# Optimization experiments

Hardware: AMD Instinct MI355X
Metric: run time of the kernel (lower is better)

## Reference

```python
import jax, jax.numpy as jnp
import numpy as np

T, N, NH, H, R, E = 6, 50000, 128, 4, 2, 800000
D = NH // H


def _pos_enc(d, t):
    # matches HTHGNLayer TempAttention.generate_positional_encoding
    k = np.arange(0, d, 2)
    div = np.exp(k * -np.log(100000.0) / d)
    pos = np.arange(1, t + 1)[:, None].astype(np.float64)
    pe = np.zeros((t, d), dtype=np.float32)
    pe[:, 0::2] = np.sin(pos * div)
    pe[:, 1::2] = np.cos(pos * div)
    return jnp.asarray(pe)


def setup_inputs() -> dict:
    key = jax.random.key(0)
    ks = jax.random.split(key, 16)
    s = 1.0 / np.sqrt(NH)  # keep activations / attention logits well-scaled
    inp = {
        "x": jax.random.normal(ks[0], (T, N, NH), jnp.float32),
        "src": jax.random.randint(ks[1], (R, E), 0, N, jnp.int32),
        "dst": jax.random.randint(ks[2], (R, E), 0, N, jnp.int32),
        "gat_wsrc": jax.random.normal(ks[3], (R, NH, NH), jnp.float32) * s,
        "gat_wdst": jax.random.normal(ks[4], (R, NH, NH), jnp.float32) * s,
        "gat_attn": jax.random.normal(ks[5], (R, H, D), jnp.float32) * s,
        "gat_bias": jnp.zeros((R, NH), jnp.float32),
        "h_bias": jnp.zeros((NH,), jnp.float32),
        "sem_w1": jax.random.normal(ks[6], (NH, NH), jnp.float32) * s,
        "sem_b1": jnp.zeros((NH,), jnp.float32),
        "sem_w2": jax.random.normal(ks[7], (NH,), jnp.float32) * s,
        "proj_w": jax.random.normal(ks[8], (NH, NH), jnp.float32) * s,
        "proj_b": jnp.zeros((NH,), jnp.float32),
        "qw": jax.random.normal(ks[9], (NH, NH), jnp.float32) * s,
        "kw": jax.random.normal(ks[10], (NH, NH), jnp.float32) * s,
        "vw": jax.random.normal(ks[11], (NH, NH), jnp.float32) * s,
        "fc_w": jax.random.normal(ks[12], (NH, NH), jnp.float32) * s,
        "fc_b": jnp.zeros((NH,), jnp.float32),
        "res_w": jax.random.normal(ks[13], (NH, NH), jnp.float32) * s,
        "res_b": jnp.zeros((NH,), jnp.float32),
        "res_alpha": jax.random.normal(ks[14], (1,), jnp.float32),
        "ln_gamma": jnp.ones((NH,), jnp.float32),
        "ln_beta": jnp.zeros((NH,), jnp.float32),
    }
    return inp


def _gatv2_rel(xt, s_, d_, wsrc, wdst, attn, bias):
    # one relation, one timestep: DGL GATv2Conv (share_weights=False, slope 0.2)
    fs = (xt @ wsrc).reshape(N, H, D)  # fc_src
    fd = (xt @ wdst).reshape(N, H, D)  # fc_dst
    e = jax.nn.leaky_relu(fs[s_] + fd[d_], 0.2)           # [E,H,D]
    sc = jnp.einsum('ehd,hd->eh', e, attn)                # [E,H]
    m = jax.ops.segment_max(sc, d_, num_segments=N)       # edge softmax per dst
    ex = jnp.exp(sc - m[d_])
    den = jax.ops.segment_sum(ex, d_, num_segments=N)
    alpha = ex / den[d_]
    out = jax.ops.segment_sum(alpha[:, :, None] * fs[s_], d_, num_segments=N)
    return out + bias.reshape(1, H, D)                    # [N,H,D]


def reference(x, src, dst, gat_wsrc, gat_wdst, gat_attn, gat_bias, h_bias,
              sem_w1, sem_b1, sem_w2, proj_w, proj_b, qw, kw, vw, fc_w, fc_b,
              res_w, res_b, res_alpha, ln_gamma, ln_beta):
    gat_all = jax.vmap(_gatv2_rel, in_axes=(None, 0, 0, 0, 0, 0, 0))
    inter = []
    for t in range(T):  # fixed small time window
        hr = gat_all(x[t], src, dst, gat_wsrc, gat_wdst, gat_attn, gat_bias)  # [R,N,H,D]
        h = jnp.transpose(hr, (1, 0, 2, 3)).reshape(N, R, NH)  # stack + flatten heads
        # semantic attention over relations (_rel_agg)
        w = jnp.tanh(h @ sem_w1 + sem_b1) @ sem_w2             # [N,R]
        beta = jax.nn.softmax(w.mean(0), axis=0)               # [R]
        hsem = jax.nn.relu(jnp.einsum('r,nrd->nd', beta, h))
        inter.append(jax.nn.relu(hsem + h_bias))               # _apply: bias + relu
    inter = jnp.stack(inter, 0)                                # [T,N,NH]
    # temporal self-attention (TempAttention, no 1/sqrt(d) scaling -- faithful)
    pe = _pos_enc(NH, T)
    xt = jnp.transpose(inter, (1, 0, 2))                       # [N,T,NH]
    hh = xt @ proj_w + proj_b + pe
    q, k, v = hh @ qw, hh @ kw, hh @ vw
    sc = jax.nn.softmax(jnp.einsum('ntd,nsd->nts', q, k), axis=-1)
    ho = jax.nn.relu(jnp.einsum('nts,nsd->ntd', sc, v) @ fc_w + fc_b)
    ho = jnp.transpose(ho, (1, 0, 2))                          # [T,N,NH]
    # gated residual + LayerNorm
    a = jax.nn.sigmoid(res_alpha)[0]
    out = ho * a + (x @ res_w + res_b) * (1.0 - a)
    mu = out.mean(-1, keepdims=True)
    var = out.var(-1, keepdims=True)
    return (out - mu) / jnp.sqrt(var + 1e-5) * ln_gamma + ln_beta
```

## Files before the change

kernel.cpp:

```cpp
#include <hip/hip_runtime.h>
#include <math.h>

#define T_  6
#define N_  50000
#define NH_ 128
#define R_  2
#define E_  800000
#define SEMW_BLOCKS ((2*N_ + 127)/128)

typedef __attribute__((ext_vector_type(8))) short bf16x8;
typedef __attribute__((ext_vector_type(4))) float f32x4;

__device__ inline unsigned short f2b(float f) {
    union { float f; unsigned int u; } v; v.f = f;
    unsigned int u = v.u;
    unsigned int r = (u + 0x7FFFu + ((u >> 16) & 1u)) >> 16;
    return (unsigned short)r;
}
__device__ inline float b2f(unsigned short h) {
    union { unsigned int u; float f; } v; v.u = ((unsigned int)h) << 16;
    return v.f;
}

__global__ void hist_kernel(const int* __restrict__ dst, int* __restrict__ counts) {
    int j = blockIdx.x * blockDim.x + threadIdx.x;
    if (j < R_ * E_) atomicAdd(&counts[(j / E_) * N_ + dst[j]], 1);
}

__global__ __launch_bounds__(1024) void scan_kernel(const int* __restrict__ counts,
                                                    int* __restrict__ offsets,
                                                    int* __restrict__ cursor) {
    int r = blockIdx.x;
    __shared__ int sm[1024];
    __shared__ int carry;
    if (threadIdx.x == 0) carry = 0;
    __syncthreads();
    for (int base = 0; base < N_; base += 1024) {
        int i = base + threadIdx.x;
        int v = (i < N_) ? counts[r * N_ + i] : 0;
        sm[threadIdx.x] = v;
        __syncthreads();
        for (int off = 1; off < 1024; off <<= 1) {
            int t = 0;
            if (threadIdx.x >= off) t = sm[threadIdx.x - off];
            __syncthreads();
            sm[threadIdx.x] += t;
            __syncthreads();
        }
        int incl = sm[threadIdx.x];
        int run = carry;
        int excl = run + incl - v;
        if (i < N_) { offsets[r * (N_ + 1) + i] = excl; cursor[r * N_ + i] = excl; }
        __syncthreads();
        if (threadIdx.x == 1023) carry = run + incl;
        __syncthreads();
    }
    if (threadIdx.x == 0) offsets[r * (N_ + 1) + N_] = carry;
}

__global__ void scatter_kernel(const int* __restrict__ src, const int* __restrict__ dst,
                               int* __restrict__ cursor, int* __restrict__ srcs_sorted) {
    int j = blockIdx.x * blockDim.x + threadIdx.x;
    if (j < R_ * E_) {
        int r = j / E_;
        int pos = atomicAdd(&cursor[r * N_ + dst[j]], 1);
        srcs_sorted[(size_t)r * E_ + pos] = src[j];
    }
}

__global__ void pe_kernel(float* __restrict__ pe) {
    int c = threadIdx.x;
    int k = c & ~1;
    double div = exp((double)k * (-log(100000.0) / 128.0));
    for (int t = 0; t < T_; t++) {
        double pos = (double)(t + 1);
        double v = (c & 1) ? cos(pos * div) : sin(pos * div);
        pe[t * NH_ + c] = (float)v;
    }
}

__global__ void cvt_x_kernel(const float* __restrict__ in, unsigned short* __restrict__ out, long n) {
    long i = ((long)blockIdx.x * blockDim.x + threadIdx.x) * 8;
    if (i >= n) return;
    float4 a = *(const float4*)(in + i);
    float4 b = *(const float4*)(in + i + 4);
    union { unsigned short s[8]; uint4 u; } o;
    o.s[0] = f2b(a.x); o.s[1] = f2b(a.y); o.s[2] = f2b(a.z); o.s[3] = f2b(a.w);
    o.s[4] = f2b(b.x); o.s[5] = f2b(b.y); o.s[6] = f2b(b.z); o.s[7] = f2b(b.w);
    *(uint4*)(out + i) = o.u;
}

struct CvtArgs {
    const float* s[6];
    unsigned short* d[6];
};
__global__ void cvt_wt_kernel(CvtArgs a) {
    int y = blockIdx.y, n = blockIdx.x, k = threadIdx.x;
    a.d[y][n * 128 + k] = f2b(a.s[y][k * 128 + n]);
}

__global__ void build_m_kernel(const float* __restrict__ qw, const float* __restrict__ kw,
                               const float* __restrict__ vw, const float* __restrict__ fcw,
                               float* __restrict__ Mu, float* __restrict__ Mwv) {
    int y = blockIdx.y, c = blockIdx.x, f = threadIdx.x;
    float s = 0.f;
    if (y == 0) {
        for (int d = 0; d < 128; d++) s += kw[f * 128 + d] * qw[c * 128 + d];
        Mu[c * 128 + f] = s;
    } else {
        for (int d = 0; d < 128; d++) s += vw[f * 128 + d] * fcw[d * 128 + c];
        Mwv[c * 128 + f] = s;
    }
}

__global__ void fold_w_kernel(const float* __restrict__ proj, const float* __restrict__ Mu,
                              const float* __restrict__ Mwv, unsigned short* __restrict__ wt_hh,
                              unsigned short* __restrict__ wt_pu, unsigned short* __restrict__ wt_pwv) {
    int y = blockIdx.y, c = blockIdx.x, k = threadIdx.x;
    if (y == 0) { wt_hh[c * 128 + k] = f2b(proj[k * 128 + c]); return; }
    const float* M = (y == 1) ? Mu : Mwv;
    float s = 0.f;
    for (int f = 0; f < 128; f++) s += proj[k * 128 + f] * M[c * 128 + f];
    ((y == 1) ? wt_pu : wt_pwv)[c * 128 + k] = f2b(s);
}

__global__ void fold_c_kernel(const float* __restrict__ proj_b, const float* __restrict__ pe,
                              const float* __restrict__ Mu, const float* __restrict__ Mwv,
                              const float* __restrict__ res_b, float* __restrict__ cbuf) {
    int t = blockIdx.x, c = threadIdx.x;
    cbuf[0 * 768 + t * 128 + c] = proj_b[c] + pe[t * 128 + c];
    float s1 = 0.f, s2 = 0.f;
    for (int f = 0; f < 128; f++) {
        float b = proj_b[f] + pe[t * 128 + f];
        s1 += b * Mu[c * 128 + f];
        s2 += b * Mwv[c * 128 + f];
    }
    cbuf[1 * 768 + t * 128 + c] = s1;
    cbuf[2 * 768 + t * 128 + c] = s2;
    cbuf[3 * 768 + t * 128 + c] = res_b[c];
}

struct MArgs {
    const unsigned short* A;
    const unsigned short* Axb;
    const unsigned short* W0; const unsigned short* W1;
    const unsigned short* W2; const unsigned short* W3;
    unsigned short* C0; unsigned short* C1; unsigned short* C2; unsigned short* C3;
    const float* cb;
    long row0;
    int  M;
};

template <int EPI>
__global__ __launch_bounds__(256) void mgemm_kernel(MArgs g) {
    __shared__ __align__(16) char As[128 * 256];
    __shared__ __align__(16) char Bs[128 * 256];
    int tid = threadIdx.x;
    int brow0 = blockIdx.x * 128;
    const unsigned short* Ws[4] = {g.W0, g.W1, g.W2, g.W3};
    unsigned short* Cs[4] = {g.C0, g.C1, g.C2, g.C3};

    auto stageA = [&](const unsigned short* Abase, bool m1) {
#pragma unroll
        for (int i = 0; i < 8; i++) {
            int c = tid + i * 256;
            int row = c >> 4;
            int cb = (c & 15) << 4;
            int scb = cb ^ ((row & 7) << 4);
            int grow = brow0 + row;
            float4 av = make_float4(0.f, 0.f, 0.f, 0.f);
            if (grow < g.M) {
                long ar;
                if (!m1) ar = grow;
                else { long gg = g.row0 + grow; long n = gg / 6, t = gg - n * 6; ar = t * (long)N_ + n; }
                av = *(const float4*)((const char*)Abase + ar * 256 + cb);
            }
            *(float4*)(As + row * 256 + scb) = av;
        }
    };
    auto stageB = [&](const unsigned short* W) {
#pragma unroll
        for (int i = 0; i < 8; i++) {
            int c = tid + i * 256;
            int row = c >> 4;
            int cb = (c & 15) << 4;
            int scb = cb ^ ((row & 7) << 4);
            *(float4*)(Bs + row * 256 + scb) = *(const float4*)((const char*)W + (size_t)row * 256 + cb);
        }
    };

    int w = tid >> 6, l = tid & 63;
    int l15 = l & 15, lg = l >> 4;

    stageA(g.A, false);
    for (int y = 0; y < 4; y++) {
        if (y > 0) __syncthreads();
        if (EPI == 3 && y == 3) stageA(g.Axb, true);
        stageB(Ws[y]);
        __syncthreads();

        f32x4 acc[2][8];
#pragma unroll
        for (int a = 0; a < 2; a++)
#pragma unroll
            for (int b = 0; b < 8; b++) acc[a][b] = (f32x4)(0.f);
#pragma unroll
        for (int ks = 0; ks < 4; ks++) {
            bf16x8 bf[8];
#pragma unroll
            for (int nt = 0; nt < 8; nt++) {
                int rn = nt * 16 + l15;
                int cbyte = (ks * 64 + lg * 16) ^ ((rn & 7) << 4);
                bf[nt] = *(const bf16x8*)(Bs + rn * 256 + cbyte);
            }
#pragma unroll
            for (int mt = 0; mt < 2; mt++) {
                int rm = w * 32 + mt * 16 + l15;
                int cbyte = (ks * 64 + lg * 16) ^ ((rm & 7) << 4);
                bf16x8 af = *(const bf16x8*)(As + rm * 256 + cbyte);
#pragma unroll
                for (int nt = 0; nt < 8; nt++)
                    acc[mt][nt] = __builtin_amdgcn_mfma_f32_16x16x32_bf16(af, bf[nt], acc[mt][nt], 0, 0, 0);
            }
        }
        unsigned short* C = Cs[y];
#pragma unroll
        for (int mt = 0; mt < 2; mt++) {
#pragma unroll
            for (int r = 0; r < 4; r++) {
                int row = w * 32 + mt * 16 + lg * 4 + r;
                int grow = brow0 + row;
                if (grow >= g.M) continue;
                long t6 = 0;
                if (EPI == 3) t6 = (g.row0 + grow) % 6;
#pragma unroll
                for (int nt = 0; nt < 8; nt++) {
                    int col = nt * 16 + l15;
                    float v = acc[mt][nt][r];
                    if (EPI == 3) v += g.cb[y * 768 + t6 * 128 + col];
                    C[(size_t)grow * 128 + col] = f2b(v);
                }
            }
        }
    }
}

__global__ __launch_bounds__(256) void semw_kernel(const unsigned short* __restrict__ Abase,
                                                   const unsigned short* __restrict__ Wt,
                                                   const float* __restrict__ b1,
                                                   const float* __restrict__ w2,
                                                   float* __restrict__ partials) {
    __shared__ __align__(16) char As[128 * 256];
    __shared__ __align__(16) char Bs[128 * 256];
    __shared__ float bs[2];
    int tid = threadIdx.x;
    if (tid < 2) bs[tid] = 0.f;
    int tl = blockIdx.y;
    const unsigned short* A = Abase + (size_t)tl * N_ * 256;
    const int M = 2 * N_;
    int brow0 = blockIdx.x * 128;
#pragma unroll
    for (int i = 0; i < 8; i++) {
        int c = tid + i * 256;
        int row = c >> 4;
        int cb = (c & 15) << 4;
        int scb = cb ^ ((row & 7) << 4);
        *(float4*)(Bs + row * 256 + scb) = *(const float4*)((const char*)Wt + (size_t)row * 256 + cb);
        int grow = brow0 + row;
        float4 av = make_float4(0.f, 0.f, 0.f, 0.f);
        if (grow < M) av = *(const float4*)((const char*)A + (size_t)grow * 256 + cb);
        *(float4*)(As + row * 256 + scb) = av;
    }
    __syncthreads();
    int w = tid >> 6, l = tid & 63;
    int l15 = l & 15, lg = l >> 4;
    f32x4 acc[2][8];
#pragma unroll
    for (int a = 0; a < 2; a++)
#pragma unroll
        for (int b = 0; b < 8; b++) acc[a][b] = (f32x4)(0.f);
#pragma unroll
    for (int ks = 0; ks < 4; ks++) {
        bf16x8 bf[8];
#pragma unroll
        for (int nt = 0; nt < 8; nt++) {
            int rn = nt * 16 + l15;
            int cbyte = (ks * 64 + lg * 16) ^ ((rn & 7) << 4);
            bf[nt] = *(const bf16x8*)(Bs + rn * 256 + cbyte);
        }
#pragma unroll
        for (int mt = 0; mt < 2; mt++) {
            int rm = w * 32 + mt * 16 + l15;
            int cbyte = (ks * 64 + lg * 16) ^ ((rm & 7) << 4);
            bf16x8 af = *(const bf16x8*)(As + rm * 256 + cbyte);
#pragma unroll
            for (int nt = 0; nt < 8; nt++)
                acc[mt][nt] = __builtin_amdgcn_mfma_f32_16x16x32_bf16(af, bf[nt], acc[mt][nt], 0, 0, 0);
        }
    }
#pragma unroll
    for (int mt = 0; mt < 2; mt++) {
#pragma unroll
        for (int r = 0; r < 4; r++) {
            int row = w * 32 + mt * 16 + lg * 4 + r;
            int grow = brow0 + row;
            float s = 0.f;
#pragma unroll
            for (int nt = 0; nt < 8; nt++) {
                int col = nt * 16 + l15;
                s += tanhf(acc[mt][nt][r] + b1[col]) * w2[col];
            }
#pragma unroll
            for (int mask = 1; mask <= 8; mask <<= 1) s += __shfl_xor(s, mask);
            if (l15 == 0 && grow < M) atomicAdd(&bs[grow & 1], s);
        }
    }
    __syncthreads();
    if (tid < 2) partials[((size_t)tl * SEMW_BLOCKS + blockIdx.x) * 2 + tid] = bs[tid];
}

__global__ __launch_bounds__(512) void beta_kernel(const float* __restrict__ partials,
                                                   float* __restrict__ beta2) {
    int t = blockIdx.x;
    const float* p = partials + (size_t)t * SEMW_BLOCKS * 2;
    float s0 = 0.f, s1 = 0.f;
    for (int i = threadIdx.x; i < SEMW_BLOCKS; i += 512) { s0 += p[i * 2]; s1 += p[i * 2 + 1]; }
#pragma unroll
    for (int mask = 1; mask <= 32; mask <<= 1) { s0 += __shfl_xor(s0, mask); s1 += __shfl_xor(s1, mask); }
    __shared__ float w0[8], w1[8];
    int w = threadIdx.x >> 6;
    if ((threadIdx.x & 63) == 0) { w0[w] = s0; w1[w] = s1; }
    __syncthreads();
    if (threadIdx.x == 0) {
        float t0 = 0.f, t1 = 0.f;
        for (int i = 0; i < 8; i++) { t0 += w0[i]; t1 += w1[i]; }
        float m0 = t0 / (float)N_, m1 = t1 / (float)N_;
        float mx = fmaxf(m0, m1);
        float e0 = __expf(m0 - mx), e1 = __expf(m1 - mx);
        float inv = 1.f / (e0 + e1);
        beta2[t * 2] = e0 * inv; beta2[t * 2 + 1] = e1 * inv;
    }
}

__global__ __launch_bounds__(256) void gat_edge_kernel(const unsigned short* __restrict__ R0,
                                                       const int* __restrict__ offsets,
                                                       const int* __restrict__ srcs_sorted,
                                                       const float* __restrict__ gat_attn,
                                                       const float* __restrict__ gat_bias,
                                                       unsigned short* __restrict__ hbuf, int TB) {
    int y = blockIdx.y;
    int r = y & 1, tl = y >> 1;
    const unsigned short* fs = R0 + ((size_t)(2 * r) * TB + tl) * N_ * 128;
    const unsigned short* fd = R0 + ((size_t)(2 * r + 1) * TB + tl) * N_ * 128;
    unsigned short* hout = hbuf + (size_t)tl * N_ * 256;
    const int* offs = offsets + r * (N_ + 1);
    const int* srcs = srcs_sorted + (size_t)r * E_;
    int lane = threadIdx.x & 63;
    int q = lane >> 4, l16 = lane & 15;
    int c0 = l16 * 8;
    int wid = (blockIdx.x * blockDim.x + threadIdx.x) >> 6;
    int nw = (gridDim.x * blockDim.x) >> 6;
    float4 a0 = *(const float4*)(gat_attn + r * 128 + c0);
    float4 a1 = *(const float4*)(gat_attn + r * 128 + c0 + 4);
    float av[8] = {a0.x, a0.y, a0.z, a0.w, a1.x, a1.y, a1.z, a1.w};
    float4 bb0 = *(const float4*)(gat_bias + r * 128 + c0);
    float4 bb1 = *(const float4*)(gat_bias + r * 128 + c0 + 4);
    float bv[8] = {bb0.x, bb0.y, bb0.z, bb0.w, bb1.x, bb1.y, bb1.z, bb1.w};

    for (int gidx = wid; gidx < N_ / 4; gidx += nw) {
        int n = gidx * 4 + q;
        uint4 fdp = *(const uint4*)(fd + (size_t)n * 128 + c0);
        const unsigned int* fdu = (const unsigned int*)&fdp;
        float fdv[8];
#pragma unroll
        for (int j = 0; j < 8; j++)
            fdv[j] = (j & 1) ? b2f((unsigned short)(fdu[j >> 1] >> 16)) : b2f((unsigned short)fdu[j >> 1]);
        int e0 = offs[n], e1 = offs[n + 1];
        int deg = e1 - e0;
        int m = deg;
        m = max(m, __shfl_xor(m, 16));
        m = max(m, __shfl_xor(m, 32));
        float den = 0.f;
        float acc[8];
#pragma unroll
        for (int j = 0; j < 8; j++) acc[j] = 0.f;

        uint4 fp = make_uint4(0, 0, 0, 0);
        if (deg > 0) fp = *(const uint4*)(fs + (size_t)srcs[e0] * 128 + c0);
        for (int i = 0; i < m; i++) {
            uint4 nxt = make_uint4(0, 0, 0, 0);
            if (i + 1 < deg) nxt = *(const uint4*)(fs + (size_t)srcs[e0 + i + 1] * 128 + c0);
            const unsigned int* fu = (const unsigned int*)&fp;
            float f[8];
            float v = 0.f;
#pragma unroll
            for (int j = 0; j < 8; j++) {
                f[j] = (j & 1) ? b2f((unsigned short)(fu[j >> 1] >> 16)) : b2f((unsigned short)fu[j >> 1]);
                float t = f[j] + fdv[j];
                float lr = fmaf(0.2f, fminf(t, 0.f), fmaxf(t, 0.f));
                v = fmaf(av[j], lr, v);
            }
            v += __int_as_float(__builtin_amdgcn_ds_swizzle(__float_as_int(v), 0x041F));
            v += __int_as_float(__builtin_amdgcn_ds_swizzle(__float_as_int(v), 0x081F));
            float p = (i < deg) ? __expf(v) : 0.f;
            den += p;
#pragma unroll
            for (int j = 0; j < 8; j++) acc[j] = fmaf(p, f[j], acc[j]);
            fp = nxt;
        }
        float inv = (deg > 0) ? 1.f / den : 0.f;
        union { unsigned short s[8]; uint4 u; } o;
#pragma unroll
        for (int j = 0; j < 8; j++) o.s[j] = f2b(fmaf(acc[j], inv, bv[j]));
        *(uint4*)(hout + (size_t)(n * 2 + r) * 128 + c0) = o.u;
    }
}

__global__ void hsem_kernel(const unsigned short* __restrict__ hbuf, const float* __restrict__ beta2,
                            const float* __restrict__ h_bias, unsigned short* __restrict__ inter,
                            int tbase) {
    int idx = blockIdx.x * blockDim.x + threadIdx.x;
    if (idx >= N_ * 16) return;
    int tl = blockIdx.y;
    int t = tbase + tl;
    const unsigned short* h = hbuf + (size_t)tl * N_ * 256;
    int n = idx >> 4, c8 = (idx & 15) * 8;
    float b0 = beta2[tl * 2], b1 = beta2[tl * 2 + 1];
    uint4 x0 = *(const uint4*)(h + (size_t)n * 256 + c8);
    uint4 x1 = *(const uint4*)(h + (size_t)n * 256 + 128 + c8);
    const unsigned int* p0 = (const unsigned int*)&x0;
    const unsigned int* p1 = (const unsigned int*)&x1;
    float4 hb0 = *(const float4*)(h_bias + c8);
    float4 hb1 = *(const float4*)(h_bias + c8 + 4);
    float hbv[8] = {hb0.x, hb0.y, hb0.z, hb0.w, hb1.x, hb1.y, hb1.z, hb1.w};
    union { unsigned short s[8]; uint4 u; } o;
#pragma unroll
    for (int i = 0; i < 8; i++) {
        unsigned short s0 = (i & 1) ? (unsigned short)(p0[i >> 1] >> 16) : (unsigned short)p0[i >> 1];
        unsigned short s1 = (i & 1) ? (unsigned short)(p1[i >> 1] >> 16) : (unsigned short)p1[i >> 1];
        float z = fmaxf(fmaxf(b0 * b2f(s0) + b1 * b2f(s1), 0.f) + hbv[i], 0.f);
        o.s[i] = f2b(z);
    }
    *(uint4*)(inter + ((size_t)n * 6 + t) * 128 + c8) = o.u;
}

__global__ __launch_bounds__(256) void temporal_kernel(const unsigned short* __restrict__ hh,
                                                       const unsigned short* __restrict__ uu,
                                                       const unsigned short* __restrict__ wvv,
                                                       const unsigned short* __restrict__ rv,
                                                       const float* __restrict__ fc_b,
                                                       const float* __restrict__ res_alpha,
                                                       const float* __restrict__ ln_g,
                                                       const float* __restrict__ ln_b,
                                                       float* __restrict__ out, long n0, int nNodes) {
    int lane = threadIdx.x & 63;
    int wid = (blockIdx.x * blockDim.x + threadIdx.x) >> 6;
    if (wid >= nNodes) return;
    long n = n0 + wid;
    size_t base = (size_t)wid * 6 * 128 + 2 * lane;
    float h2[6][2], u2[6][2], wv2[6][2], rv2[6][2];
#pragma unroll
    for (int t = 0; t < 6; t++) {
        unsigned int hp = *(const unsigned int*)(hh + base + t * 128);
        h2[t][0] = b2f((unsigned short)hp); h2[t][1] = b2f((unsigned short)(hp >> 16));
        unsigned int up = *(const unsigned int*)(uu + base + t * 128);
        u2[t][0] = b2f((unsigned short)up); u2[t][1] = b2f((unsigned short)(up >> 16));
        unsigned int wp = *(const unsigned int*)(wvv + base + t * 128);
        wv2[t][0] = b2f((unsigned short)wp); wv2[t][1] = b2f((unsigned short)(wp >> 16));
        unsigned int rp = *(const unsigned int*)(rv + base + t * 128);
        rv2[t][0] = b2f((unsigned short)rp); rv2[t][1] = b2f((unsigned short)(rp >> 16));
    }
    float sc[6][6];
#pragma unroll
    for (int t = 0; t < 6; t++)
#pragma unroll
        for (int s = 0; s < 6; s++)
            sc[t][s] = h2[t][0] * u2[s][0] + h2[t][1] * u2[s][1];
#pragma unroll
    for (int mask = 1; mask <= 32; mask <<= 1)
#pragma unroll
        for (int t = 0; t < 6; t++)
#pragma unroll
            for (int s = 0; s < 6; s++)
                sc[t][s] += __shfl_xor(sc[t][s], mask);

    float a = 1.f / (1.f + __expf(-res_alpha[0]));
    float2 fb = ((const float2*)fc_b)[lane];
    float2 lg = ((const float2*)ln_g)[lane];
    float2 lb = ((const float2*)ln_b)[lane];
#pragma unroll
    for (int t = 0; t < 6; t++) {
        float mx = sc[t][0];
#pragma unroll
        for (int s = 1; s < 6; s++) mx = fmaxf(mx, sc[t][s]);
        float p[6]; float den = 0.f;
#pragma unroll
        for (int s = 0; s < 6; s++) { p[s] = __expf(sc[t][s] - mx); den += p[s]; }
        float inv = 1.f / den;
        float ox = 0.f, oy = 0.f;
#pragma unroll
        for (int s = 0; s < 6; s++) { ox += p[s] * wv2[s][0]; oy += p[s] * wv2[s][1]; }
        ox = fmaxf(ox * inv + fb.x, 0.f);
        oy = fmaxf(oy * inv + fb.y, 0.f);
        ox = ox * a + rv2[t][0] * (1.f - a);
        oy = oy * a + rv2[t][1] * (1.f - a);
        float s1 = ox + oy, s2 = ox * ox + oy * oy;
#pragma unroll
        for (int mask = 1; mask <= 32; mask <<= 1) {
            s1 += __shfl_xor(s1, mask);
            s2 += __shfl_xor(s2, mask);
        }
        float mu = s1 * (1.f / 128.f);
        float var = s2 * (1.f / 128.f) - mu * mu;
        float rs = rsqrtf(var + 1e-5f);
        float2 o;
        o.x = (ox - mu) * rs * lg.x + lb.x;
        o.y = (oy - mu) * rs * lg.y + lb.y;
        ((float2*)(out + ((size_t)t * N_ + n) * 128))[lane] = o;
    }
}

extern "C" void kernel_launch(void* const* d_in, const int* in_sizes, int n_in,
                              void* d_out, int out_size, void* d_ws, size_t ws_size,
                              hipStream_t stream) {
    const float* x        = (const float*)d_in[0];
    const int*   src      = (const int*)d_in[1];
    const int*   dst      = (const int*)d_in[2];
    const float* gat_wsrc = (const float*)d_in[3];
    const float* gat_wdst = (const float*)d_in[4];
    const float* gat_attn = (const float*)d_in[5];
    const float* gat_bias = (const float*)d_in[6];
    const float* h_bias   = (const float*)d_in[7];
    const float* sem_w1   = (const float*)d_in[8];
    const float* sem_b1   = (const float*)d_in[9];
    const float* sem_w2   = (const float*)d_in[10];
    const float* proj_w   = (const float*)d_in[11];
    const float* proj_b   = (const float*)d_in[12];
    const float* qw       = (const float*)d_in[13];
    const float* kw       = (const float*)d_in[14];
    const float* vw       = (const float*)d_in[15];
    const float* fc_w     = (const float*)d_in[16];
    const float* fc_b     = (const float*)d_in[17];
    const float* res_w    = (const float*)d_in[18];
    const float* res_b    = (const float*)d_in[19];
    const float* res_alpha= (const float*)d_in[20];
    const float* ln_g     = (const float*)d_in[21];
    const float* ln_b     = (const float*)d_in[22];
    (void)in_sizes; (void)n_in; (void)out_size;

    int TB = (ws_size >= (size_t)500 * 1024 * 1024) ? 6 : 2;
    int CH = (TB == 6) ? N_ : 12500;

    char* ws = (char*)d_ws;
    size_t off = 0;
    auto alloc = [&](size_t bytes) -> void* {
        void* p = ws + off;
        off += (bytes + 255) & ~(size_t)255;
        return p;
    };
    int*   counts      = (int*)alloc((size_t)R_ * N_ * 4);
    int*   offsets     = (int*)alloc((size_t)R_ * (N_ + 1) * 4);
    int*   cursor      = (int*)alloc((size_t)R_ * N_ * 4);
    int*   srcs_sorted = (int*)alloc((size_t)R_ * E_ * 4);
    float* pe          = (float*)alloc(T_ * NH_ * 4);
    float* partials    = (float*)alloc((size_t)T_ * SEMW_BLOCKS * 2 * 4);
    float* beta2       = (float*)alloc(T_ * 2 * 4);
    float* Mu          = (float*)alloc(16384 * 4);
    float* Mwv         = (float*)alloc(16384 * 4);
    float* cbuf        = (float*)alloc(4 * 768 * 4);
    unsigned short* wt_gs0  = (unsigned short*)alloc(16384 * 2);
    unsigned short* wt_gs1  = (unsigned short*)alloc(16384 * 2);
    unsigned short* wt_gd0  = (unsigned short*)alloc(16384 * 2);
    unsigned short* wt_gd1  = (unsigned short*)alloc(16384 * 2);
    unsigned short* wt_sem  = (unsigned short*)alloc(16384 * 2);
    unsigned short* wt_res  = (unsigned short*)alloc(16384 * 2);
    unsigned short* wt_hh   = (unsigned short*)alloc(16384 * 2);
    unsigned short* wt_pu   = (unsigned short*)alloc(16384 * 2);
    unsigned short* wt_pwv  = (unsigned short*)alloc(16384 * 2);
    unsigned short* xb      = (unsigned short*)alloc((size_t)T_ * N_ * 128 * 2);
    unsigned short* inter   = (unsigned short*)alloc((size_t)N_ * T_ * 128 * 2);
    size_t Rgat = (size_t)4 * TB * N_ * 128 * 2;
    size_t Rtmp = (size_t)4 * CH * 6 * 128 * 2;
    unsigned short* R0      = (unsigned short*)alloc(Rgat > Rtmp ? Rgat : Rtmp);

    unsigned short* hbuf = (unsigned short*)d_out;

    hipMemsetAsync(counts, 0, (size_t)R_ * N_ * 4, stream);
    hist_kernel<<<(R_ * E_ + 255) / 256, 256, 0, stream>>>(dst, counts);
    scan_kernel<<<R_, 1024, 0, stream>>>(counts, offsets, cursor);
    scatter_kernel<<<(R_ * E_ + 255) / 256, 256, 0, stream>>>(src, dst, cursor, srcs_sorted);
    pe_kernel<<<1, 128, 0, stream>>>(pe);
    cvt_x_kernel<<<18750, 256, 0, stream>>>(x, xb, (long)T_ * N_ * 128);
    CvtArgs ca;
    ca.s[0] = gat_wsrc;         ca.d[0] = wt_gs0;
    ca.s[1] = gat_wsrc + 16384; ca.d[1] = wt_gs1;
    ca.s[2] = gat_wdst;         ca.d[2] = wt_gd0;
    ca.s[3] = gat_wdst + 16384; ca.d[3] = wt_gd1;
    ca.s[4] = sem_w1;           ca.d[4] = wt_sem;
    ca.s[5] = res_w;            ca.d[5] = wt_res;
    cvt_wt_kernel<<<dim3(128, 6), 128, 0, stream>>>(ca);
    build_m_kernel<<<dim3(128, 2), 128, 0, stream>>>(qw, kw, vw, fc_w, Mu, Mwv);
    fold_w_kernel<<<dim3(128, 3), 128, 0, stream>>>(proj_w, Mu, Mwv, wt_hh, wt_pu, wt_pwv);
    fold_c_kernel<<<6, 128, 0, stream>>>(proj_b, pe, Mu, Mwv, res_b, cbuf);

    size_t TBN = (size_t)TB * N_ * 128;
    for (int tg = 0; tg < T_ / TB; tg++) {
        int tbase = tg * TB;
        MArgs ga{};
        ga.A = xb + (size_t)tbase * N_ * 128;
        ga.row0 = 0; ga.M = TB * N_;
        ga.W0 = wt_gs0; ga.C0 = R0;
        ga.W1 = wt_gd0; ga.C1 = R0 + TBN;
        ga.W2 = wt_gs1; ga.C2 = R0 + 2 * TBN;
        ga.W3 = wt_gd1; ga.C3 = R0 + 3 * TBN;
        mgemm_kernel<0><<<dim3((TB * N_ + 127) / 128, 1), 256, 0, stream>>>(ga);

        gat_edge_kernel<<<dim3(1024, 2 * TB), 256, 0, stream>>>(R0, offsets, srcs_sorted,
                                                                gat_attn, gat_bias, hbuf, TB);

        semw_kernel<<<dim3(SEMW_BLOCKS, TB), 256, 0, stream>>>(hbuf, wt_sem, sem_b1, sem_w2,
                                                               partials + (size_t)tbase * SEMW_BLOCKS * 2);
        beta_kernel<<<TB, 512, 0, stream>>>(partials + (size_t)tbase * SEMW_BLOCKS * 2,
                                            beta2 + tbase * 2);
        hsem_kernel<<<dim3((N_ * 16 + 255) / 256, TB), 256, 0, stream>>>(hbuf, beta2 + tbase * 2,
                                                                         h_bias, inter, tbase);
    }

    for (int c = 0; c < N_ / CH; c++) {
        long n0 = (long)c * CH;
        long r0 = n0 * 6;
        int Mc = CH * 6;
        int nb = (Mc + 127) / 128;
        size_t MB = (size_t)Mc * 128;

        MArgs gt{};
        gt.A = inter + (size_t)r0 * 128;
        gt.Axb = xb;
        gt.row0 = r0; gt.M = Mc; gt.cb = cbuf;
        gt.W0 = wt_hh;  gt.C0 = R0;
        gt.W1 = wt_pu;  gt.C1 = R0 + MB;
        gt.W2 = wt_pwv; gt.C2 = R0 + 2 * MB;
        gt.W3 = wt_res; gt.C3 = R0 + 3 * MB;
        mgemm_kernel<3><<<dim3(nb, 1), 256, 0, stream>>>(gt);

        temporal_kernel<<<(CH + 3) / 4, 256, 0, stream>>>(R0, R0 + MB, R0 + 2 * MB, R0 + 3 * MB,
                                                          fc_b, res_alpha, ln_g, ln_b,
                                                          (float*)d_out, n0, CH);
    }
}
```

Before: 1.425 ms.

## Sort destination nodes by in-degree for GAT edge load balance and pack float2 math

```diff
diff --git a/kernel.cpp b/kernel.cpp
--- a/kernel.cpp
+++ b/kernel.cpp
@@ -10,6 +10,7 @@
 
 typedef __attribute__((ext_vector_type(8))) short bf16x8;
 typedef __attribute__((ext_vector_type(4))) float f32x4;
+typedef __attribute__((ext_vector_type(2))) float f32x2;
 
 __device__ inline unsigned short f2b(float f) {
     union { float f; unsigned int u; } v; v.f = f;
@@ -20,6 +21,11 @@
 __device__ inline float b2f(unsigned short h) {
     union { unsigned int u; float f; } v; v.u = ((unsigned int)h) << 16;
     return v.f;
+}
+__device__ inline f32x2 up2(unsigned int u) {
+    union { unsigned int ui; float f; } lo, hi;
+    lo.ui = u << 16; hi.ui = u & 0xffff0000u;
+    f32x2 r; r.x = lo.f; r.y = hi.f; return r;
 }
 
 __global__ void hist_kernel(const int* __restrict__ dst, int* __restrict__ counts) {
@@ -68,6 +74,42 @@
     }
 }
 
+__global__ void dhist_kernel(const int* __restrict__ counts, int* __restrict__ dh) {
+    int j = blockIdx.x * blockDim.x + threadIdx.x;
+    if (j < R_ * N_) {
+        int r = j / N_;
+        int d = counts[j]; d = d < 1023 ? d : 1023;
+        atomicAdd(&dh[r * 1024 + d], 1);
+    }
+}
+
+__global__ __launch_bounds__(1024) void dscan_kernel(const int* __restrict__ dh, int* __restrict__ dcur) {
+    int r = blockIdx.x;
+    __shared__ int sm[1024];
+    int v = dh[r * 1024 + threadIdx.x];
+    sm[threadIdx.x] = v;
+    __syncthreads();
+    for (int off = 1; off < 1024; off <<= 1) {
+        int t = 0;
+        if (threadIdx.x >= off) t = sm[threadIdx.x - off];
+        __syncthreads();
+        sm[threadIdx.x] += t;
+        __syncthreads();
+    }
+    dcur[r * 1024 + threadIdx.x] = sm[threadIdx.x] - v;
+}
+
+__global__ void dperm_kernel(const int* __restrict__ counts, int* __restrict__ dcur,
+                             int* __restrict__ perm) {
+    int j = blockIdx.x * blockDim.x + threadIdx.x;
+    if (j < R_ * N_) {
+        int r = j / N_, n = j - r * N_;
+        int d = counts[j]; d = d < 1023 ? d : 1023;
+        int pos = atomicAdd(&dcur[r * 1024 + d], 1);
+        perm[r * N_ + pos] = n;
+    }
+}
+
 __global__ void pe_kernel(float* __restrict__ pe) {
     int c = threadIdx.x;
     int k = c & ~1;
@@ -345,6 +387,7 @@
 __global__ __launch_bounds__(256) void gat_edge_kernel(const unsigned short* __restrict__ R0,
                                                        const int* __restrict__ offsets,
                                                        const int* __restrict__ srcs_sorted,
+                                                       const int* __restrict__ perm,
                                                        const float* __restrict__ gat_attn,
                                                        const float* __restrict__ gat_bias,
                                                        unsigned short* __restrict__ hbuf, int TB) {
@@ -355,35 +398,40 @@
     unsigned short* hout = hbuf + (size_t)tl * N_ * 256;
     const int* offs = offsets + r * (N_ + 1);
     const int* srcs = srcs_sorted + (size_t)r * E_;
+    const int* pm = perm + r * N_;
     int lane = threadIdx.x & 63;
     int q = lane >> 4, l16 = lane & 15;
     int c0 = l16 * 8;
     int wid = (blockIdx.x * blockDim.x + threadIdx.x) >> 6;
     int nw = (gridDim.x * blockDim.x) >> 6;
-    float4 a0 = *(const float4*)(gat_attn + r * 128 + c0);
-    float4 a1 = *(const float4*)(gat_attn + r * 128 + c0 + 4);
-    float av[8] = {a0.x, a0.y, a0.z, a0.w, a1.x, a1.y, a1.z, a1.w};
-    float4 bb0 = *(const float4*)(gat_bias + r * 128 + c0);
-    float4 bb1 = *(const float4*)(gat_bias + r * 128 + c0 + 4);
-    float bv[8] = {bb0.x, bb0.y, bb0.z, bb0.w, bb1.x, bb1.y, bb1.z, bb1.w};
+    f32x2 av2[4], bv2[4];
+    {
+        float4 a0 = *(const float4*)(gat_attn + r * 128 + c0);
+        float4 a1 = *(const float4*)(gat_attn + r * 128 + c0 + 4);
+        av2[0].x = a0.x; av2[0].y = a0.y; av2[1].x = a0.z; av2[1].y = a0.w;
+        av2[2].x = a1.x; av2[2].y = a1.y; av2[3].x = a1.z; av2[3].y = a1.w;
+        float4 b0 = *(const float4*)(gat_bias + r * 128 + c0);
+        float4 b1 = *(const float4*)(gat_bias + r * 128 + c0 + 4);
+        bv2[0].x = b0.x; bv2[0].y = b0.y; bv2[1].x = b0.z; bv2[1].y = b0.w;
+        bv2[2].x = b1.x; bv2[2].y = b1.y; bv2[3].x = b1.z; bv2[3].y = b1.w;
+    }
 
     for (int gidx = wid; gidx < N_ / 4; gidx += nw) {
-        int n = gidx * 4 + q;
+        int n = pm[gidx * 4 + q];
         uint4 fdp = *(const uint4*)(fd + (size_t)n * 128 + c0);
         const unsigned int* fdu = (const unsigned int*)&fdp;
-        float fdv[8];
-#pragma unroll
-        for (int j = 0; j < 8; j++)
-            fdv[j] = (j & 1) ? b2f((unsigned short)(fdu[j >> 1] >> 16)) : b2f((unsigned short)fdu[j >> 1]);
+        f32x2 fdv[4];
+#pragma unroll
+        for (int k = 0; k < 4; k++) fdv[k] = up2(fdu[k]);
         int e0 = offs[n], e1 = offs[n + 1];
         int deg = e1 - e0;
         int m = deg;
         m = max(m, __shfl_xor(m, 16));
         m = max(m, __shfl_xor(m, 32));
         float den = 0.f;
-        float acc[8];
-#pragma unroll
-        for (int j = 0; j < 8; j++) acc[j] = 0.f;
+        f32x2 acc[4];
+#pragma unroll
+        for (int k = 0; k < 4; k++) acc[k] = (f32x2)(0.f);
 
         uint4 fp = make_uint4(0, 0, 0, 0);
         if (deg > 0) fp = *(const uint4*)(fs + (size_t)srcs[e0] * 128 + c0);
@@ -391,27 +439,33 @@
             uint4 nxt = make_uint4(0, 0, 0, 0);
             if (i + 1 < deg) nxt = *(const uint4*)(fs + (size_t)srcs[e0 + i + 1] * 128 + c0);
             const unsigned int* fu = (const unsigned int*)&fp;
-            float f[8];
-            float v = 0.f;
-#pragma unroll
-            for (int j = 0; j < 8; j++) {
-                f[j] = (j & 1) ? b2f((unsigned short)(fu[j >> 1] >> 16)) : b2f((unsigned short)fu[j >> 1]);
-                float t = f[j] + fdv[j];
-                float lr = fmaf(0.2f, fminf(t, 0.f), fmaxf(t, 0.f));
-                v = fmaf(av[j], lr, v);
+            f32x2 f[4];
+            f32x2 vv = (f32x2)(0.f);
+#pragma unroll
+            for (int k = 0; k < 4; k++) {
+                f[k] = up2(fu[k]);
+                f32x2 t = f[k] + fdv[k];
+                f32x2 lr = __builtin_elementwise_max(t, (f32x2)(0.f))
+                         + 0.2f * __builtin_elementwise_min(t, (f32x2)(0.f));
+                vv += av2[k] * lr;
             }
+            float v = vv.x + vv.y;
             v += __int_as_float(__builtin_amdgcn_ds_swizzle(__float_as_int(v), 0x041F));
             v += __int_as_float(__builtin_amdgcn_ds_swizzle(__float_as_int(v), 0x081F));
             float p = (i < deg) ? __expf(v) : 0.f;
             den += p;
-#pragma unroll
-            for (int j = 0; j < 8; j++) acc[j] = fmaf(p, f[j], acc[j]);
+            f32x2 pv; pv.x = p; pv.y = p;
+#pragma unroll
+            for (int k = 0; k < 4; k++) acc[k] += pv * f[k];
             fp = nxt;
         }
         float inv = (deg > 0) ? 1.f / den : 0.f;
         union { unsigned short s[8]; uint4 u; } o;
 #pragma unroll
-        for (int j = 0; j < 8; j++) o.s[j] = f2b(fmaf(acc[j], inv, bv[j]));
+        for (int k = 0; k < 4; k++) {
+            o.s[2 * k]     = f2b(fmaf(acc[k].x, inv, bv2[k].x));
+            o.s[2 * k + 1] = f2b(fmaf(acc[k].y, inv, bv2[k].y));
+        }
         *(uint4*)(hout + (size_t)(n * 2 + r) * 128 + c0) = o.u;
     }
 }
@@ -562,6 +616,9 @@
     int*   offsets     = (int*)alloc((size_t)R_ * (N_ + 1) * 4);
     int*   cursor      = (int*)alloc((size_t)R_ * N_ * 4);
     int*   srcs_sorted = (int*)alloc((size_t)R_ * E_ * 4);
+    int*   dh          = (int*)alloc((size_t)R_ * 1024 * 4);
+    int*   dcur        = (int*)alloc((size_t)R_ * 1024 * 4);
+    int*   perm        = (int*)alloc((size_t)R_ * N_ * 4);
     float* pe          = (float*)alloc(T_ * NH_ * 4);
     float* partials    = (float*)alloc((size_t)T_ * SEMW_BLOCKS * 2 * 4);
     float* beta2       = (float*)alloc(T_ * 2 * 4);
@@ -586,9 +643,13 @@
     unsigned short* hbuf = (unsigned short*)d_out;
 
     hipMemsetAsync(counts, 0, (size_t)R_ * N_ * 4, stream);
+    hipMemsetAsync(dh, 0, (size_t)R_ * 1024 * 4, stream);
     hist_kernel<<<(R_ * E_ + 255) / 256, 256, 0, stream>>>(dst, counts);
     scan_kernel<<<R_, 1024, 0, stream>>>(counts, offsets, cursor);
     scatter_kernel<<<(R_ * E_ + 255) / 256, 256, 0, stream>>>(src, dst, cursor, srcs_sorted);
+    dhist_kernel<<<(R_ * N_ + 255) / 256, 256, 0, stream>>>(counts, dh);
+    dscan_kernel<<<R_, 1024, 0, stream>>>(dh, dcur);
+    dperm_kernel<<<(R_ * N_ + 255) / 256, 256, 0, stream>>>(counts, dcur, perm);
     pe_kernel<<<1, 128, 0, stream>>>(pe);
     cvt_x_kernel<<<18750, 256, 0, stream>>>(x, xb, (long)T_ * N_ * 128);
     CvtArgs ca;
@@ -615,7 +676,7 @@
         ga.W3 = wt_gd1; ga.C3 = R0 + 3 * TBN;
         mgemm_kernel<0><<<dim3((TB * N_ + 127) / 128, 1), 256, 0, stream>>>(ga);
 
-        gat_edge_kernel<<<dim3(1024, 2 * TB), 256, 0, stream>>>(R0, offsets, srcs_sorted,
+        gat_edge_kernel<<<dim3(1024, 2 * TB), 256, 0, stream>>>(R0, offsets, srcs_sorted, perm,
                                                                 gat_attn, gat_bias, hbuf, TB);
 
         semw_kernel<<<dim3(SEMW_BLOCKS, TB), 256, 0, stream>>>(hbuf, wt_sem, sem_b1, sem_w2,
```

New measurement: 1.699 ms. +19.2%, slower.

## Parallelize CSR scan across blocks, prescale source offsets, simplify leaky-relu attention

Applied to the files above, without the earlier changes.

```diff
diff --git a/kernel.cpp b/kernel.cpp
--- a/kernel.cpp
+++ b/kernel.cpp
@@ -7,6 +7,7 @@
 #define R_  2
 #define E_  800000
 #define SEMW_BLOCKS ((2*N_ + 127)/128)
+#define NCHUNK 49
 
 typedef __attribute__((ext_vector_type(8))) short bf16x8;
 typedef __attribute__((ext_vector_type(4))) float f32x4;
@@ -27,35 +28,51 @@
     if (j < R_ * E_) atomicAdd(&counts[(j / E_) * N_ + dst[j]], 1);
 }
 
-__global__ __launch_bounds__(1024) void scan_kernel(const int* __restrict__ counts,
-                                                    int* __restrict__ offsets,
-                                                    int* __restrict__ cursor) {
-    int r = blockIdx.x;
+__global__ __launch_bounds__(1024) void scan1_kernel(const int* __restrict__ counts,
+                                                     int* __restrict__ lexcl,
+                                                     int* __restrict__ csums) {
+    int r = blockIdx.y, c = blockIdx.x;
+    int i = c * 1024 + threadIdx.x;
+    int v = (i < N_) ? counts[r * N_ + i] : 0;
     __shared__ int sm[1024];
-    __shared__ int carry;
-    if (threadIdx.x == 0) carry = 0;
+    sm[threadIdx.x] = v;
     __syncthreads();
-    for (int base = 0; base < N_; base += 1024) {
-        int i = base + threadIdx.x;
-        int v = (i < N_) ? counts[r * N_ + i] : 0;
-        sm[threadIdx.x] = v;
+    for (int off = 1; off < 1024; off <<= 1) {
+        int t = 0;
+        if (threadIdx.x >= off) t = sm[threadIdx.x - off];
         __syncthreads();
-        for (int off = 1; off < 1024; off <<= 1) {
-            int t = 0;
-            if (threadIdx.x >= off) t = sm[threadIdx.x - off];
-            __syncthreads();
-            sm[threadIdx.x] += t;
-            __syncthreads();
-        }
-        int incl = sm[threadIdx.x];
-        int run = carry;
-        int excl = run + incl - v;
-        if (i < N_) { offsets[r * (N_ + 1) + i] = excl; cursor[r * N_ + i] = excl; }
+        sm[threadIdx.x] += t;
         __syncthreads();
-        if (threadIdx.x == 1023) carry = run + incl;
-        __syncthreads();
-    }
-    if (threadIdx.x == 0) offsets[r * (N_ + 1) + N_] = carry;
+    }
+    if (i < N_) lexcl[r * N_ + i] = sm[threadIdx.x] - v;
+    if (threadIdx.x == 1023) csums[r * 64 + c] = sm[1023];
+}
+
+__global__ void scan2_kernel(int* __restrict__ csums, int* __restrict__ offsets) {
+    int r = threadIdx.x >> 6, l = threadIdx.x & 63;
+    if (r < R_) {
+        int v = (l < NCHUNK) ? csums[r * 64 + l] : 0;
+        int s = v;
+        for (int off = 1; off < 64; off <<= 1) {
+            int t = __shfl_up(s, off);
+            if (l >= off) s += t;
+        }
+        if (l < NCHUNK) csums[r * 64 + l] = s - v;
+        if (l == NCHUNK - 1) offsets[r * (N_ + 1) + N_] = s;
+    }
+}
+
+__global__ __launch_bounds__(1024) void scan3_kernel(const int* __restrict__ lexcl,
+                                                     const int* __restrict__ csums,
+                                                     int* __restrict__ offsets,
+                                                     int* __restrict__ cursor) {
+    int r = blockIdx.y;
+    int i = blockIdx.x * 1024 + threadIdx.x;
+    if (i < N_) {
+        int o = lexcl[r * N_ + i] + csums[r * 64 + blockIdx.x];
+        offsets[r * (N_ + 1) + i] = o;
+        cursor[r * N_ + i] = o;
+    }
 }
 
 __global__ void scatter_kernel(const int* __restrict__ src, const int* __restrict__ dst,
@@ -64,7 +81,7 @@
     if (j < R_ * E_) {
         int r = j / E_;
         int pos = atomicAdd(&cursor[r * N_ + dst[j]], 1);
-        srcs_sorted[(size_t)r * E_ + pos] = src[j];
+        srcs_sorted[(size_t)r * E_ + pos] = src[j] << 8;
     }
 }
 
@@ -350,7 +367,7 @@
                                                        unsigned short* __restrict__ hbuf, int TB) {
     int y = blockIdx.y;
     int r = y & 1, tl = y >> 1;
-    const unsigned short* fs = R0 + ((size_t)(2 * r) * TB + tl) * N_ * 128;
+    const char* fsb = (const char*)(R0 + ((size_t)(2 * r) * TB + tl) * N_ * 128);
     const unsigned short* fd = R0 + ((size_t)(2 * r + 1) * TB + tl) * N_ * 128;
     unsigned short* hout = hbuf + (size_t)tl * N_ * 256;
     const int* offs = offsets + r * (N_ + 1);
@@ -358,6 +375,7 @@
     int lane = threadIdx.x & 63;
     int q = lane >> 4, l16 = lane & 15;
     int c0 = l16 * 8;
+    const char* fsc = fsb + c0 * 2;
     int wid = (blockIdx.x * blockDim.x + threadIdx.x) >> 6;
     int nw = (gridDim.x * blockDim.x) >> 6;
     float4 a0 = *(const float4*)(gat_attn + r * 128 + c0);
@@ -386,22 +404,25 @@
         for (int j = 0; j < 8; j++) acc[j] = 0.f;
 
         uint4 fp = make_uint4(0, 0, 0, 0);
-        if (deg > 0) fp = *(const uint4*)(fs + (size_t)srcs[e0] * 128 + c0);
+        if (deg > 0) fp = *(const uint4*)(fsc + srcs[e0]);
         for (int i = 0; i < m; i++) {
             uint4 nxt = make_uint4(0, 0, 0, 0);
-            if (i + 1 < deg) nxt = *(const uint4*)(fs + (size_t)srcs[e0 + i + 1] * 128 + c0);
+            if (i + 1 < deg) nxt = *(const uint4*)(fsc + srcs[e0 + i + 1]);
             const unsigned int* fu = (const unsigned int*)&fp;
             float f[8];
-            float v = 0.f;
+            float vlin = 0.f, vabs = 0.f;
 #pragma unroll
             for (int j = 0; j < 8; j++) {
                 f[j] = (j & 1) ? b2f((unsigned short)(fu[j >> 1] >> 16)) : b2f((unsigned short)fu[j >> 1]);
                 float t = f[j] + fdv[j];
-                float lr = fmaf(0.2f, fminf(t, 0.f), fmaxf(t, 0.f));
-                v = fmaf(av[j], lr, v);
+                vlin = fmaf(av[j], t, vlin);
+                vabs = fmaf(av[j], fabsf(t), vabs);
             }
-            v += __int_as_float(__builtin_amdgcn_ds_swizzle(__float_as_int(v), 0x041F));
-            v += __int_as_float(__builtin_amdgcn_ds_swizzle(__float_as_int(v), 0x081F));
+            vlin += __int_as_float(__builtin_amdgcn_ds_swizzle(__float_as_int(vlin), 0x041F));
+            vabs += __int_as_float(__builtin_amdgcn_ds_swizzle(__float_as_int(vabs), 0x041F));
+            vlin += __int_as_float(__builtin_amdgcn_ds_swizzle(__float_as_int(vlin), 0x081F));
+            vabs += __int_as_float(__builtin_amdgcn_ds_swizzle(__float_as_int(vabs), 0x081F));
+            float v = fmaf(0.4f, vabs, 0.6f * vlin);
             float p = (i < deg) ? __expf(v) : 0.f;
             den += p;
 #pragma unroll
@@ -562,6 +583,8 @@
     int*   offsets     = (int*)alloc((size_t)R_ * (N_ + 1) * 4);
     int*   cursor      = (int*)alloc((size_t)R_ * N_ * 4);
     int*   srcs_sorted = (int*)alloc((size_t)R_ * E_ * 4);
+    int*   lexcl       = (int*)alloc((size_t)R_ * N_ * 4);
+    int*   csums       = (int*)alloc((size_t)R_ * 64 * 4);
     float* pe          = (float*)alloc(T_ * NH_ * 4);
     float* partials    = (float*)alloc((size_t)T_ * SEMW_BLOCKS * 2 * 4);
     float* beta2       = (float*)alloc(T_ * 2 * 4);
@@ -587,7 +610,9 @@
 
     hipMemsetAsync(counts, 0, (size_t)R_ * N_ * 4, stream);
     hist_kernel<<<(R_ * E_ + 255) / 256, 256, 0, stream>>>(dst, counts);
-    scan_kernel<<<R_, 1024, 0, stream>>>(counts, offsets, cursor);
+    scan1_kernel<<<dim3(NCHUNK, R_), 1024, 0, stream>>>(counts, lexcl, csums);
+    scan2_kernel<<<1, 128, 0, stream>>>(csums, offsets);
+    scan3_kernel<<<dim3(NCHUNK, R_), 1024, 0, stream>>>(lexcl, csums, offsets, cursor);
     scatter_kernel<<<(R_ * E_ + 255) / 256, 256, 0, stream>>>(src, dst, cursor, srcs_sorted);
     pe_kernel<<<1, 128, 0, stream>>>(pe);
     cvt_x_kernel<<<18750, 256, 0, stream>>>(x, xb, (long)T_ * N_ * 128);
```

Result: faster. 1.336 ms (-6.2%).
